# Performance work log

Hardware: AMD Instinct MI355X
Metric: run time of the kernel (lower is better)

Reference implementation:

```python
import jax, jax.numpy as jnp
import numpy as np

VOCAB = 50257
CUTOFF = (10000, 50000, 50257)  # cutoff + [vocab_size] per __init__
D = 1024
B, T = 2, 1024
HEAD_SZ = CUTOFF[0] + 2  # cutoff[0] + n_tail_clusters


def setup_inputs() -> dict:
    key = jax.random.key(0)
    ks = jax.random.split(key, 7)
    def xavier(k, shp):
        # xavier_uniform as in init_weights
        bound = np.sqrt(6.0 / (shp[0] + shp[1])).astype(np.float32)
        return jax.random.uniform(k, shp, dtype=jnp.float32, minval=-bound, maxval=bound)
    return {
        "input": jax.random.normal(ks[0], (B, T, D), dtype=jnp.float32),
        "target": jax.random.randint(ks[1], (B, T), 0, VOCAB),
        "head_w": xavier(ks[2], (HEAD_SZ, D)),              # [10002, 1024]
        "t0_a": xavier(ks[3], (D, D)),                       # [1024, 1024]
        "t0_b": xavier(ks[4], (CUTOFF[1] - CUTOFF[0], D)),   # [40000, 1024]
        "t1_a": xavier(ks[5], (D // 4, D)),                  # [256, 1024]
        "t1_b": xavier(ks[6], (CUTOFF[2] - CUTOFF[1], D // 4)),  # [207, 256]
    }


def reference(input, target, head_w, t0_a, t0_b, t1_a, t1_b):
    # Faithful jax version of AdaptiveSoftmax.get_log_prob (eval mode, dropout=0).
    # Torch updates log_probs[idxs, start:end] only for rows whose target lies in
    # cluster i (leaving other rows zero); we express the same gather->small GEMM
    # chain->log_softmax->prior-add->scatter via masked writes (jit-friendly).
    bsz, length, dim = input.shape
    xi = input.reshape(-1, dim)                     # [N, D]
    tgt = target.reshape(-1)                        # [N]

    head_lp = jax.nn.log_softmax(xi @ head_w.T, axis=1)        # [N, HEAD_SZ]
    tail_priors = head_lp[:, CUTOFF[0] - 1:HEAD_SZ - 1]        # [N, 2]

    log_probs = jnp.zeros((xi.shape[0], VOCAB), dtype=input.dtype)
    log_probs = log_probs.at[:, :HEAD_SZ].set(head_lp)

    tails = ((t0_a, t0_b), (t1_a, t1_b))
    for i, (wa, wb) in enumerate(tails):
        lo, hi = CUTOFF[i], CUTOFF[i + 1]
        mask = (tgt >= lo) & (tgt < hi)                        # [N]
        # Linear(D, D//4**i) -> Linear(D//4**i, hi-lo), then log_softmax + prior
        tail_lp = jax.nn.log_softmax((xi @ wa.T) @ wb.T, axis=1) + tail_priors[:, i:i + 1]
        log_probs = log_probs.at[:, lo:hi].set(
            jnp.where(mask[:, None], tail_lp, log_probs[:, lo:hi]))
    return log_probs.reshape(bsz, length, VOCAB)
```

## Files before the change

kernel.cpp:

```cpp
#include <hip/hip_runtime.h>

typedef unsigned short u16;
typedef unsigned int u32;
typedef __attribute__((ext_vector_type(4))) float f32x4;
typedef __bf16 bf16x8 __attribute__((ext_vector_type(8)));
typedef __attribute__((ext_vector_type(8))) unsigned short u16x8;

__device__ __forceinline__ u16 f2bf(float x) {
    u32 u = __builtin_bit_cast(u32, x);
    u += 0x7FFFu + ((u >> 16) & 1u);
    return (u16)(u >> 16);
}
__device__ __forceinline__ float bf2f(u16 u) {
    return __builtin_bit_cast(float, ((u32)u) << 16);
}
__device__ __forceinline__ void gld_lds16(void* lds, const void* g) {
    __builtin_amdgcn_global_load_lds(
        (const __attribute__((address_space(1))) void*)g,
        (__attribute__((address_space(3))) void*)lds, 16, 0, 0);
}
__device__ __forceinline__ void merge_ms(float& m, float& s, float mo, float so) {
    float mn = fmaxf(m, mo);
    s = s * __expf(m - mn) + so * __expf(mo - mn);
    m = mn;
}
__device__ __forceinline__ void wave_reduce_ms(float& m, float& s) {
#pragma unroll
    for (int off = 32; off; off >>= 1) {
        float mo = __shfl_xor(m, off);
        float so = __shfl_xor(s, off);
        merge_ms(m, s, mo, so);
    }
}
__device__ __forceinline__ void block_reduce_ms(float& m, float& s, float* red, int tid) {
    wave_reduce_ms(m, s);
    __syncthreads();
    if ((tid & 63) == 0) { red[(tid >> 6) * 2] = m; red[(tid >> 6) * 2 + 1] = s; }
    __syncthreads();
    float M = red[0], S = red[1];
#pragma unroll
    for (int w = 1; w < 4; w++) merge_ms(M, S, red[w * 2], red[w * 2 + 1]);
    m = M; s = S;
}

__device__ __forceinline__ size_t pack_base_u16(long row) {
    return (size_t)row * 100514 + 59936 - ((row * 2) & 7);
}

__global__ __launch_bounds__(256) void cvt_kernel(const float* __restrict__ src,
                                                  u16* __restrict__ dst, int n) {
    int idx = blockIdx.x * blockDim.x + threadIdx.x;
    int stride = gridDim.x * blockDim.x;
    for (int i = idx * 4; i < n; i += stride * 4) {
        float4 v = *(const float4*)(src + i);
        ushort4 o;
        o.x = f2bf(v.x); o.y = f2bf(v.y); o.z = f2bf(v.z); o.w = f2bf(v.w);
        *(ushort4*)(dst + i) = o;
    }
}

__global__ __launch_bounds__(256) void build_map(const int* __restrict__ tgt,
                                                 int* __restrict__ rowlist,
                                                 int* __restrict__ cntbuf) {
    __shared__ int cs[257];
    __shared__ int fu[256];
    int t = threadIdx.x;
    int cnt_local = 0, first_un = 1 << 30;
    int mk[8];
#pragma unroll
    for (int k = 0; k < 8; k++) {
        int r = t * 8 + k;
        int tg = tgt[r];
        int m = (tg >= 10000 && tg < 50000) ? 1 : 0;
        mk[k] = m;
        cnt_local += m;
        if (!m && first_un == (1 << 30)) first_un = r;
    }
    cs[t + 1] = cnt_local;
    fu[t] = first_un;
    __syncthreads();
    if (t == 0) {
        cs[0] = 0;
        for (int i = 1; i <= 256; i++) cs[i] += cs[i - 1];
        int d = 1 << 30;
        for (int i = 0; i < 256; i++) d = min(d, fu[i]);
        if (d == (1 << 30)) d = 0;
        int cnt = cs[256];
        cntbuf[0] = cnt;
        cntbuf[1] = (cnt + 255) & ~255;
        cntbuf[2] = d;
    }
    __syncthreads();
    int off = cs[t];
#pragma unroll
    for (int k = 0; k < 8; k++)
        if (mk[k]) rowlist[off++] = t * 8 + k;
    int cnt = cs[256], cntp = (cnt + 255) & ~255, d = cntbuf[2];
    for (int j = cnt + t; j < cntp; j += 256) rowlist[j] = d;
}

template <int MODE>
__global__ __launch_bounds__(256) void gemm_nt(const u16* __restrict__ A, int lda,
                                               const u16* __restrict__ B, int ldb,
                                               float* __restrict__ C, u16* __restrict__ Cb,
                                               long ldc, long c_off, int K) {
    __shared__ u16 lA[128 * 32];
    __shared__ u16 lB[128 * 32];
    const int tid = threadIdx.x;
    const int lane = tid & 63, wv = tid >> 6;
    const int m0 = blockIdx.x * 128, n0 = blockIdx.y * 128;

    const u16* gA0 = A + (size_t)(m0 + (tid >> 2)) * lda + (tid & 3) * 8;
    const u16* gB0 = B + (size_t)(n0 + (tid >> 2)) * ldb + (tid & 3) * 8;
    char* dA = (char*)lA + wv * 1024;
    char* dB = (char*)lB + wv * 1024;

    f32x4 acc[4][4] = {};
    const int wm = wv >> 1, wn = wv & 1;
    const int lr = lane & 15;
    const int lk = (lane >> 4) * 8;

    for (int kt = 0; kt < K; kt += 32) {
        __syncthreads();
        gld_lds16(dA, gA0);
        gld_lds16(dA + 4096, gA0 + 64 * (size_t)lda);
        gld_lds16(dB, gB0);
        gld_lds16(dB + 4096, gB0 + 64 * (size_t)ldb);
        gA0 += 32; gB0 += 32;
        __syncthreads();

        bf16x8 af[4], bfr[4];
#pragma unroll
        for (int i = 0; i < 4; i++) {
            af[i]  = *(const bf16x8*)(lA + (wm * 64 + i * 16 + lr) * 32 + lk);
            bfr[i] = *(const bf16x8*)(lB + (wn * 64 + i * 16 + lr) * 32 + lk);
        }
#pragma unroll
        for (int i = 0; i < 4; i++)
#pragma unroll
            for (int j = 0; j < 4; j++)
                acc[i][j] = __builtin_amdgcn_mfma_f32_16x16x32_bf16(af[i], bfr[j], acc[i][j], 0, 0, 0);
    }

    const int cr = (lane >> 4) * 4;
    const int cc = lane & 15;
#pragma unroll
    for (int i = 0; i < 4; i++) {
        int rbase = m0 + wm * 64 + i * 16 + cr;
#pragma unroll
        for (int j = 0; j < 4; j++) {
            int c = n0 + wn * 64 + j * 16 + cc;
#pragma unroll
            for (int q = 0; q < 4; q++) {
                size_t r = (size_t)(rbase + q);
                if (MODE == 1) Cb[r * (size_t)ldc + c] = f2bf(acc[i][j][q]);
                else           C[r * (size_t)ldc + (size_t)c_off + c] = acc[i][j][q];
            }
        }
    }
}

__global__ __launch_bounds__(512, 2) void gemm256_t0(const u16* __restrict__ PROJ,
                                                     const u16* __restrict__ B,
                                                     u16* __restrict__ Cb,
                                                     const int* __restrict__ rowlist,
                                                     const int* __restrict__ cntbuf,
                                                     float* __restrict__ part) {
    const int m0 = blockIdx.x * 256, n0 = blockIdx.y * 256;
    if (m0 >= cntbuf[1]) return;
    __shared__ u16 lds[4][16384];
    const int tid = threadIdx.x;
    const int lane = tid & 63, wv = tid >> 6;
    const int wm = wv >> 2, wn = wv & 3;
    const int lr = lane & 15, hi = lane >> 4;

    const int koff = (tid & 7) * 8;
    const int rit = tid >> 3;
    const u16* srcA[4];
    const u16* srcB[4];
#pragma unroll
    for (int p = 0; p < 4; p++) {
        srcA[p] = PROJ + (size_t)rowlist[m0 + p * 64 + rit] * 1280 + koff;
        srcB[p] = B + (size_t)(n0 + p * 64 + rit) * 1024 + koff;
    }

    f32x4 acc[8][4] = {};

    auto stage = [&](int buf, int kt) {
        u16* dA = &lds[buf * 2 + 0][0] + tid * 8;
        u16* dB = &lds[buf * 2 + 1][0] + tid * 8;
#pragma unroll
        for (int p = 0; p < 4; p++) {
            gld_lds16(dA + p * 4096, srcA[p] + kt);
            gld_lds16(dB + p * 4096, srcB[p] + kt);
        }
    };
    auto compute = [&](int buf) {
        const u16* lA = &lds[buf * 2 + 0][0];
        const u16* lB = &lds[buf * 2 + 1][0];
        bf16x8 bfr[4][2];
#pragma unroll
        for (int j = 0; j < 4; j++)
#pragma unroll
            for (int ks = 0; ks < 2; ks++)
                bfr[j][ks] = *(const bf16x8*)(lB + (wn * 64 + j * 16 + lr) * 64 + ks * 32 + hi * 8);
#pragma unroll
        for (int m = 0; m < 8; m++) {
            bf16x8 a0 = *(const bf16x8*)(lA + (wm * 128 + m * 16 + lr) * 64 + hi * 8);
            bf16x8 a1 = *(const bf16x8*)(lA + (wm * 128 + m * 16 + lr) * 64 + 32 + hi * 8);
#pragma unroll
            for (int j = 0; j < 4; j++) {
                acc[m][j] = __builtin_amdgcn_mfma_f32_16x16x32_bf16(a0, bfr[j][0], acc[m][j], 0, 0, 0);
                acc[m][j] = __builtin_amdgcn_mfma_f32_16x16x32_bf16(a1, bfr[j][1], acc[m][j], 0, 0, 0);
            }
        }
    };

    stage(0, 0);
    __syncthreads();
    int cur = 0;
#pragma unroll 1
    for (int t = 0; t < 15; ++t) {
        stage(cur ^ 1, (t + 1) * 64);
        compute(cur);
        __syncthreads();
        cur ^= 1;
    }
    compute(cur);

    const int cr = hi * 4, cc = lr;
#pragma unroll
    for (int m = 0; m < 8; m++) {
#pragma unroll
        for (int q = 0; q < 4; q++) {
            int r = m0 + wm * 128 + m * 16 + cr + q;
            long orow = rowlist[r];
            u16* dst = Cb + pack_base_u16(orow) + n0 + wn * 64 + cc;
            float s = 0.f;
#pragma unroll
            for (int j = 0; j < 4; j++) {
                float v = acc[m][j][q];
                dst[j * 16] = f2bf(v);
                s += __expf(v);
            }
            s += __shfl_xor(s, 1); s += __shfl_xor(s, 2);
            s += __shfl_xor(s, 4); s += __shfl_xor(s, 8);
            if (cc == 0) part[(size_t)r * 628 + (n0 >> 6) + wn] = s;
        }
    }
}

__global__ __launch_bounds__(256) void head_softmax(float* __restrict__ out,
                                                    float* __restrict__ stats) {
    const int row = blockIdx.x, tid = threadIdx.x;
    float* p = out + (size_t)row * 50257;
    __shared__ float sm[10002];
    __shared__ float red[16];
    float m = -3.4e38f, s = 0.f;
    for (int c = tid; c < 10002; c += 256) {
        float x = p[c];
        sm[c] = x;
        float m2 = fmaxf(m, x);
        s = s * __expf(m - m2) + __expf(x - m2);
        m = m2;
    }
    block_reduce_ms(m, s, red, tid);
    float A = m + __logf(s);
    for (int c = tid; c < 10002; c += 256) p[c] = sm[c] - A;
    if (tid == 0) {
        float* st = stats + row * 8;
        st[0] = sm[9999] - A;
        st[1] = sm[10000] - A;
        st[2] = sm[10000] - A;
        st[3] = sm[10001] - A;
    }
}

__global__ __launch_bounds__(256) void reduce_t0(const float* __restrict__ part,
                                                 const int* __restrict__ rowlist,
                                                 const int* __restrict__ cntbuf,
                                                 const float* __restrict__ ST,
                                                 float* __restrict__ FA) {
    int r = blockIdx.x;
    if (r >= cntbuf[0]) return;
    int tid = threadIdx.x;
    float s = 0.f;
    for (int c = tid; c < 628; c += 256) s += part[(size_t)r * 628 + c];
#pragma unroll
    for (int o = 32; o; o >>= 1) s += __shfl_xor(s, o);
    __shared__ float red[4];
    if ((tid & 63) == 0) red[tid >> 6] = s;
    __syncthreads();
    if (tid == 0) {
        float S = red[0] + red[1] + red[2] + red[3];
        int orow = rowlist[r];
        FA[orow] = __logf(S) - ST[orow * 8 + 0];
    }
}

__global__ __launch_bounds__(256) void tail0_norm(float* __restrict__ out,
                                                  const int* __restrict__ tgt,
                                                  const float* __restrict__ ST,
                                                  const float* __restrict__ FA) {
    const int row = blockIdx.x, tid = threadIdx.x;
    float* p = out + (size_t)row * 50257 + 10000;
    int t = tgt[row];
    if (t >= 10000 && t < 50000) {
        float A = FA[row];
        const u16* src = (const u16*)out + pack_base_u16(row);
        for (int k = 0; k < 5; k++) {
            float v[4][8];
#pragma unroll
            for (int g = 0; g < 4; g++) {
                int o = 2048 * g + tid * 8;
                if (o < 8000) {
                    u16x8 x = *(const u16x8*)(src + 8000 * k + o);
#pragma unroll
                    for (int z = 0; z < 8; z++) v[g][z] = bf2f(x[z]);
                }
            }
            __syncthreads();
#pragma unroll
            for (int g = 0; g < 4; g++) {
                int o = 2048 * g + tid * 8;
                if (o < 8000) {
                    int e = 8000 * k + o;
#pragma unroll
                    for (int z = 0; z < 8; z++) p[e + z] = v[g][z] - A;
                }
            }
            __syncthreads();
        }
    } else {
        float v0 = ST[row * 8 + 2], v1 = ST[row * 8 + 3];
        for (int e = tid; e < 40000; e += 256) p[e] = 0.f;
        if (tid == 0) { p[0] = v0; p[1] = v1; }
    }
}

__global__ __launch_bounds__(256) void tail1_kernel(float* __restrict__ out,
                                                    const int* __restrict__ tgt,
                                                    const u16* __restrict__ proj,
                                                    const u16* __restrict__ t1b,
                                                    const float* __restrict__ stats) {
    const int row = blockIdx.x, tid = threadIdx.x;
    float* p = out + (size_t)row * 50257 + 50000;
    int t = tgt[row];
    if (t < 50000) {
        for (int c = tid; c < 257; c += 256) p[c] = 0.f;
        return;
    }
    __shared__ float pr[256];
    __shared__ float lg[257];
    __shared__ float red[16];
    pr[tid] = bf2f(proj[(size_t)row * 1280 + 1024 + tid]);
    __syncthreads();
    for (int c = tid; c < 257; c += 256) {
        const u16* w = t1b + c * 256;
        float acc = 0.f;
        for (int k = 0; k < 256; k++) acc += bf2f(w[k]) * pr[k];
        lg[c] = acc;
    }
    __syncthreads();
    float m = -3.4e38f, s = 0.f;
    for (int c = tid; c < 257; c += 256) {
        float x = lg[c];
        float m2 = fmaxf(m, x);
        s = s * __expf(m - m2) + __expf(x - m2);
        m = m2;
    }
    block_reduce_ms(m, s, red, tid);
    float A = m + __logf(s) - stats[row * 8 + 1];
    for (int c = tid; c < 257; c += 256) p[c] = lg[c] - A;
}

#define OFF_XI    0UL
#define OFF_HEADW 4194304UL
#define OFF_TAB   24903680UL
#define OFF_T0B   27525120UL
#define OFF_T1B   109838336UL
#define OFF_PROJ  109969920UL
#define OFF_ST    115212800UL
#define OFF_PART  115278336UL
#define OFF_FA    120422912UL
#define OFF_MAP   120431104UL
#define OFF_CNT   120439296UL

extern "C" void kernel_launch(void* const* d_in, const int* in_sizes, int n_in,
                              void* d_out, int out_size, void* d_ws, size_t ws_size,
                              hipStream_t stream) {
    const float* x   = (const float*)d_in[0];
    const int*   tgt = (const int*)d_in[1];
    const float* hw  = (const float*)d_in[2];
    const float* t0a = (const float*)d_in[3];
    const float* t0b = (const float*)d_in[4];
    const float* t1a = (const float*)d_in[5];
    const float* t1b = (const float*)d_in[6];
    float* out = (float*)d_out;
    char* ws = (char*)d_ws;

    u16* XI    = (u16*)(ws + OFF_XI);
    u16* HW    = (u16*)(ws + OFF_HEADW);
    u16* TAB   = (u16*)(ws + OFF_TAB);
    u16* T0B   = (u16*)(ws + OFF_T0B);
    u16* T1B   = (u16*)(ws + OFF_T1B);
    u16* PROJ  = (u16*)(ws + OFF_PROJ);
    float* ST  = (float*)(ws + OFF_ST);
    float* PART = (float*)(ws + OFF_PART);
    float* FA  = (float*)(ws + OFF_FA);
    int* MAP   = (int*)(ws + OFF_MAP);
    int* CNT   = (int*)(ws + OFF_CNT);

    cvt_kernel<<<1024, 256, 0, stream>>>(x, XI, 2048 * 1024);
    cvt_kernel<<<2048, 256, 0, stream>>>(hw, HW, 10002 * 1024);
    cvt_kernel<<<512, 256, 0, stream>>>(t0a, TAB, 1024 * 1024);
    cvt_kernel<<<256, 256, 0, stream>>>(t1a, TAB + 1024 * 1024, 256 * 1024);
    cvt_kernel<<<2048, 256, 0, stream>>>(t0b, T0B, 40000 * 1024);
    cvt_kernel<<<64, 256, 0, stream>>>(t1b, T1B, 257 * 256);
    hipMemsetAsync(HW + 10002 * 1024, 0, 110 * 1024 * 2, stream);
    hipMemsetAsync(T0B + 40000 * 1024, 0, 192 * 1024 * 2, stream);

    build_map<<<1, 256, 0, stream>>>(tgt, MAP, CNT);

    gemm_nt<0><<<dim3(16, 79), 256, 0, stream>>>(
        XI, 1024, HW, 1024, out, nullptr, 50257L, 0L, 1024);

    head_softmax<<<2048, 256, 0, stream>>>(out, ST);

    gemm_nt<1><<<dim3(16, 10), 256, 0, stream>>>(
        XI, 1024, TAB, 1024, nullptr, PROJ, 1280L, 0L, 1024);

    gemm256_t0<<<dim3(8, 157), 512, 0, stream>>>(
        PROJ, T0B, (u16*)d_out, MAP, CNT, PART);

    reduce_t0<<<2048, 256, 0, stream>>>(PART, MAP, CNT, ST, FA);
    tail0_norm<<<2048, 256, 0, stream>>>(out, tgt, ST, FA);

    tail1_kernel<<<2048, 256, 0, stream>>>(out, tgt, PROJ, T1B, ST);
}
```

Before: 582.2 us.

## Unify GEMMs into pipelined 256-tile kernel with fused exp-sum epilogue and single convert

Merges the six fp32-to-bf16 conversion launches and two memsets into one block-partitioned kernel. Replaces the head GEMM with a templated 256x256 tile kernel that uses a 4-stage global-to-LDS pipeline and raw barriers. Its epilogue writes packed bf16 logits into the output buffer and emits partial exp-sums, so the head normalization only reads partial sums and rescales, with no online max pass. Max-free softmax can overflow if logits are large, and bf16 head logits lose precision compared with the fp32 path.

After: 558.1 us. -4.1%, faster.

```diff
diff --git a/kernel.cpp b/kernel.cpp
--- a/kernel.cpp
+++ b/kernel.cpp
@@ -19,43 +19,45 @@
         (const __attribute__((address_space(1))) void*)g,
         (__attribute__((address_space(3))) void*)lds, 16, 0, 0);
 }
-__device__ __forceinline__ void merge_ms(float& m, float& s, float mo, float so) {
-    float mn = fmaxf(m, mo);
-    s = s * __expf(m - mn) + so * __expf(mo - mn);
-    m = mn;
-}
-__device__ __forceinline__ void wave_reduce_ms(float& m, float& s) {
-#pragma unroll
-    for (int off = 32; off; off >>= 1) {
-        float mo = __shfl_xor(m, off);
-        float so = __shfl_xor(s, off);
-        merge_ms(m, s, mo, so);
-    }
-}
-__device__ __forceinline__ void block_reduce_ms(float& m, float& s, float* red, int tid) {
-    wave_reduce_ms(m, s);
-    __syncthreads();
-    if ((tid & 63) == 0) { red[(tid >> 6) * 2] = m; red[(tid >> 6) * 2 + 1] = s; }
-    __syncthreads();
-    float M = red[0], S = red[1];
-#pragma unroll
-    for (int w = 1; w < 4; w++) merge_ms(M, S, red[w * 2], red[w * 2 + 1]);
-    m = M; s = S;
-}
-
-__device__ __forceinline__ size_t pack_base_u16(long row) {
+
+__device__ __forceinline__ size_t pack_base_tail(long row) {
     return (size_t)row * 100514 + 59936 - ((row * 2) & 7);
 }
-
-__global__ __launch_bounds__(256) void cvt_kernel(const float* __restrict__ src,
-                                                  u16* __restrict__ dst, int n) {
-    int idx = blockIdx.x * blockDim.x + threadIdx.x;
-    int stride = gridDim.x * blockDim.x;
-    for (int i = idx * 4; i < n; i += stride * 4) {
-        float4 v = *(const float4*)(src + i);
-        ushort4 o;
-        o.x = f2bf(v.x); o.y = f2bf(v.y); o.z = f2bf(v.z); o.w = f2bf(v.w);
-        *(ushort4*)(dst + i) = o;
+__device__ __forceinline__ size_t pack_base_head(long row) {
+    return (size_t)row * 100514 + 20480 - ((row * 2) & 7);
+}
+
+__global__ __launch_bounds__(256) void cvt_all(const float* __restrict__ x,
+                                               const float* __restrict__ hw,
+                                               const float* __restrict__ t0a,
+                                               const float* __restrict__ t1a,
+                                               const float* __restrict__ t0b,
+                                               const float* __restrict__ t1b,
+                                               u16* __restrict__ XI, u16* __restrict__ HW,
+                                               u16* __restrict__ TAB, u16* __restrict__ T0B,
+                                               u16* __restrict__ T1B) {
+    int b = blockIdx.x;
+    const float* src; u16* dst; int n, b0, nb;
+    if (b < 80)        { src = x;    dst = XI;            n = 2097152;  b0 = 0;    nb = 80;   }
+    else if (b < 472)  { src = hw;   dst = HW;            n = 10242048; b0 = 80;   nb = 392;  }
+    else if (b < 512)  { src = t0a;  dst = TAB;           n = 1048576;  b0 = 472;  nb = 40;   }
+    else if (b < 522)  { src = t1a;  dst = TAB + 1048576; n = 262144;   b0 = 512;  nb = 10;   }
+    else if (b < 2086) { src = t0b;  dst = T0B;           n = 40960000; b0 = 522;  nb = 1564; }
+    else if (b < 2090) { src = t1b;  dst = T1B;           n = 65792;    b0 = 2086; nb = 4;    }
+    else if (b < 2100) { src = 0;    dst = HW + 10242048; n = 243712;   b0 = 2090; nb = 10;   }
+    else               { src = 0;    dst = T0B + 40960000; n = 196608;  b0 = 2100; nb = 8;    }
+    int i0 = (b - b0) * 1024 + threadIdx.x * 4;
+    int stride = nb * 1024;
+    if (src) {
+        for (int i = i0; i < n; i += stride) {
+            float4 v = *(const float4*)(src + i);
+            ushort4 o;
+            o.x = f2bf(v.x); o.y = f2bf(v.y); o.z = f2bf(v.z); o.w = f2bf(v.w);
+            *(ushort4*)(dst + i) = o;
+        }
+    } else {
+        ushort4 z = {0, 0, 0, 0};
+        for (int i = i0; i < n; i += stride) *(ushort4*)(dst + i) = z;
     }
 }
 
@@ -99,11 +101,108 @@
     for (int j = cnt + t; j < cntp; j += 256) rowlist[j] = d;
 }
 
-template <int MODE>
-__global__ __launch_bounds__(256) void gemm_nt(const u16* __restrict__ A, int lda,
-                                               const u16* __restrict__ B, int ldb,
-                                               float* __restrict__ C, u16* __restrict__ Cb,
-                                               long ldc, long c_off, int K) {
+template <int TAIL>
+__global__ __launch_bounds__(512, 2) void gemm256(const u16* __restrict__ A,
+                                                  const u16* __restrict__ B,
+                                                  u16* __restrict__ outpk,
+                                                  const int* __restrict__ rowlist,
+                                                  const int* __restrict__ cntbuf,
+                                                  float* __restrict__ part) {
+    const int m0 = blockIdx.x * 256, n0 = blockIdx.y * 256;
+    if (TAIL) { if (m0 >= cntbuf[1]) return; }
+    __shared__ u16 lds[4][16384];
+    const int tid = threadIdx.x;
+    const int lane = tid & 63, wv = tid >> 6;
+    const int wm = wv >> 2, wn = wv & 3;
+    const int lr = lane & 15, hi = lane >> 4;
+
+    const int c0 = tid, c1 = 512 + tid;
+    int ga0 = m0 + ((c0 >> 6) << 4) + (c0 & 15);
+    int ga1 = m0 + ((c1 >> 6) << 4) + (c1 & 15);
+    const u16* sA0;
+    const u16* sA1;
+    if (TAIL) {
+        sA0 = A + (size_t)rowlist[ga0] * 1280 + ((c0 >> 4) & 3) * 8;
+        sA1 = A + (size_t)rowlist[ga1] * 1280 + ((c1 >> 4) & 3) * 8;
+    } else {
+        sA0 = A + (size_t)ga0 * 1024 + ((c0 >> 4) & 3) * 8;
+        sA1 = A + (size_t)ga1 * 1024 + ((c1 >> 4) & 3) * 8;
+    }
+    const u16* sB0 = B + (size_t)(n0 + ((c0 >> 6) << 4) + (c0 & 15)) * 1024 + ((c0 >> 4) & 3) * 8;
+    const u16* sB1 = B + (size_t)(n0 + ((c1 >> 6) << 4) + (c1 & 15)) * 1024 + ((c1 >> 4) & 3) * 8;
+
+    f32x4 acc[8][4] = {};
+
+    auto stage = [&](int buf, int kt) {
+        char* d = (char*)&lds[buf][0] + tid * 16;
+        gld_lds16(d,          sA0 + kt);
+        gld_lds16(d + 8192,   sA1 + kt);
+        gld_lds16(d + 16384,  sB0 + kt);
+        gld_lds16(d + 24576,  sB1 + kt);
+    };
+    auto compute = [&](int buf) {
+        const u16* LA = &lds[buf][0];
+        const u16* LB = &lds[buf][8192];
+        bf16x8 bfr[4];
+#pragma unroll
+        for (int j = 0; j < 4; j++)
+            bfr[j] = *(const bf16x8*)(LB + (wn * 4 + j) * 512 + hi * 128 + lr * 8);
+        __builtin_amdgcn_s_setprio(1);
+#pragma unroll
+        for (int m = 0; m < 8; m++) {
+            bf16x8 af = *(const bf16x8*)(LA + (wm * 8 + m) * 512 + hi * 128 + lr * 8);
+#pragma unroll
+            for (int j = 0; j < 4; j++)
+                acc[m][j] = __builtin_amdgcn_mfma_f32_16x16x32_bf16(af, bfr[j], acc[m][j], 0, 0, 0);
+        }
+        __builtin_amdgcn_s_setprio(0);
+    };
+
+    stage(0, 0);
+    stage(1, 32);
+    asm volatile("s_waitcnt vmcnt(4)" ::: "memory");
+    __builtin_amdgcn_s_barrier();
+#pragma unroll 1
+    for (int t = 0; t < 30; ++t) {
+        stage((t + 2) & 3, (t + 2) * 32);
+        compute(t & 3);
+        asm volatile("s_waitcnt vmcnt(4)" ::: "memory");
+        __builtin_amdgcn_s_barrier();
+    }
+    compute(2);
+    asm volatile("s_waitcnt vmcnt(0)" ::: "memory");
+    __builtin_amdgcn_s_barrier();
+    compute(3);
+
+    const int cr = hi * 4, cc = lr;
+    const int climit = TAIL ? 40000 : 10002;
+    const int pstride = TAIL ? 628 : 160;
+#pragma unroll
+    for (int m = 0; m < 8; m++) {
+#pragma unroll
+        for (int q = 0; q < 4; q++) {
+            int r = m0 + wm * 128 + m * 16 + cr + q;
+            long orow = TAIL ? rowlist[r] : r;
+            size_t base = TAIL ? pack_base_tail(orow) : pack_base_head(orow);
+            u16* dst = outpk + base + n0 + wn * 64 + cc;
+            float s = 0.f;
+#pragma unroll
+            for (int j = 0; j < 4; j++) {
+                float v = acc[m][j][q];
+                dst[j * 16] = f2bf(v);
+                int col = n0 + wn * 64 + j * 16 + cc;
+                s += (col < climit) ? __expf(v) : 0.f;
+            }
+            s += __shfl_xor(s, 1); s += __shfl_xor(s, 2);
+            s += __shfl_xor(s, 4); s += __shfl_xor(s, 8);
+            if (cc == 0) part[(size_t)r * pstride + (n0 >> 6) + wn] = s;
+        }
+    }
+}
+
+__global__ __launch_bounds__(256) void gemm_nt_bf16(const u16* __restrict__ A, int lda,
+                                                    const u16* __restrict__ B, int ldb,
+                                                    u16* __restrict__ Cb, long ldc, int K) {
     __shared__ u16 lA[128 * 32];
     __shared__ u16 lB[128 * 32];
     const int tid = threadIdx.x;
@@ -151,128 +250,41 @@
         for (int j = 0; j < 4; j++) {
             int c = n0 + wn * 64 + j * 16 + cc;
 #pragma unroll
-            for (int q = 0; q < 4; q++) {
-                size_t r = (size_t)(rbase + q);
-                if (MODE == 1) Cb[r * (size_t)ldc + c] = f2bf(acc[i][j][q]);
-                else           C[r * (size_t)ldc + (size_t)c_off + c] = acc[i][j][q];
-            }
-        }
-    }
-}
-
-__global__ __launch_bounds__(512, 2) void gemm256_t0(const u16* __restrict__ PROJ,
-                                                     const u16* __restrict__ B,
-                                                     u16* __restrict__ Cb,
-                                                     const int* __restrict__ rowlist,
-                                                     const int* __restrict__ cntbuf,
-                                                     float* __restrict__ part) {
-    const int m0 = blockIdx.x * 256, n0 = blockIdx.y * 256;
-    if (m0 >= cntbuf[1]) return;
-    __shared__ u16 lds[4][16384];
-    const int tid = threadIdx.x;
-    const int lane = tid & 63, wv = tid >> 6;
-    const int wm = wv >> 2, wn = wv & 3;
-    const int lr = lane & 15, hi = lane >> 4;
-
-    const int koff = (tid & 7) * 8;
-    const int rit = tid >> 3;
-    const u16* srcA[4];
-    const u16* srcB[4];
-#pragma unroll
-    for (int p = 0; p < 4; p++) {
-        srcA[p] = PROJ + (size_t)rowlist[m0 + p * 64 + rit] * 1280 + koff;
-        srcB[p] = B + (size_t)(n0 + p * 64 + rit) * 1024 + koff;
-    }
-
-    f32x4 acc[8][4] = {};
-
-    auto stage = [&](int buf, int kt) {
-        u16* dA = &lds[buf * 2 + 0][0] + tid * 8;
-        u16* dB = &lds[buf * 2 + 1][0] + tid * 8;
-#pragma unroll
-        for (int p = 0; p < 4; p++) {
-            gld_lds16(dA + p * 4096, srcA[p] + kt);
-            gld_lds16(dB + p * 4096, srcB[p] + kt);
-        }
-    };
-    auto compute = [&](int buf) {
-        const u16* lA = &lds[buf * 2 + 0][0];
-        const u16* lB = &lds[buf * 2 + 1][0];
-        bf16x8 bfr[4][2];
-#pragma unroll
-        for (int j = 0; j < 4; j++)
-#pragma unroll
-            for (int ks = 0; ks < 2; ks++)
-                bfr[j][ks] = *(const bf16x8*)(lB + (wn * 64 + j * 16 + lr) * 64 + ks * 32 + hi * 8);
-#pragma unroll
-        for (int m = 0; m < 8; m++) {
-            bf16x8 a0 = *(const bf16x8*)(lA + (wm * 128 + m * 16 + lr) * 64 + hi * 8);
-            bf16x8 a1 = *(const bf16x8*)(lA + (wm * 128 + m * 16 + lr) * 64 + 32 + hi * 8);
-#pragma unroll
-            for (int j = 0; j < 4; j++) {
-                acc[m][j] = __builtin_amdgcn_mfma_f32_16x16x32_bf16(a0, bfr[j][0], acc[m][j], 0, 0, 0);
-                acc[m][j] = __builtin_amdgcn_mfma_f32_16x16x32_bf16(a1, bfr[j][1], acc[m][j], 0, 0, 0);
-            }
-        }
-    };
-
-    stage(0, 0);
-    __syncthreads();
-    int cur = 0;
-#pragma unroll 1
-    for (int t = 0; t < 15; ++t) {
-        stage(cur ^ 1, (t + 1) * 64);
-        compute(cur);
-        __syncthreads();
-        cur ^= 1;
-    }
-    compute(cur);
-
-    const int cr = hi * 4, cc = lr;
-#pragma unroll
-    for (int m = 0; m < 8; m++) {
-#pragma unroll
-        for (int q = 0; q < 4; q++) {
-            int r = m0 + wm * 128 + m * 16 + cr + q;
-            long orow = rowlist[r];
-            u16* dst = Cb + pack_base_u16(orow) + n0 + wn * 64 + cc;
-            float s = 0.f;
-#pragma unroll
-            for (int j = 0; j < 4; j++) {
-                float v = acc[m][j][q];
-                dst[j * 16] = f2bf(v);
-                s += __expf(v);
-            }
-            s += __shfl_xor(s, 1); s += __shfl_xor(s, 2);
-            s += __shfl_xor(s, 4); s += __shfl_xor(s, 8);
-            if (cc == 0) part[(size_t)r * 628 + (n0 >> 6) + wn] = s;
-        }
-    }
-}
-
-__global__ __launch_bounds__(256) void head_softmax(float* __restrict__ out,
-                                                    float* __restrict__ stats) {
+            for (int q = 0; q < 4; q++)
+                Cb[(size_t)(rbase + q) * (size_t)ldc + c] = f2bf(acc[i][j][q]);
+        }
+    }
+}
+
+__global__ __launch_bounds__(256) void head_norm(float* __restrict__ out,
+                                                 float* __restrict__ stats,
+                                                 const float* __restrict__ parth) {
     const int row = blockIdx.x, tid = threadIdx.x;
+    float s = (tid < 160) ? parth[(size_t)row * 160 + tid] : 0.f;
+#pragma unroll
+    for (int o = 32; o; o >>= 1) s += __shfl_xor(s, o);
+    __shared__ float red[4];
+    if ((tid & 63) == 0) red[tid >> 6] = s;
+    __syncthreads();
+    float logZ = __logf(red[0] + red[1] + red[2] + red[3]);
+    const u16* pk = (const u16*)out + pack_base_head(row);
     float* p = out + (size_t)row * 50257;
-    __shared__ float sm[10002];
-    __shared__ float red[16];
-    float m = -3.4e38f, s = 0.f;
-    for (int c = tid; c < 10002; c += 256) {
-        float x = p[c];
-        sm[c] = x;
-        float m2 = fmaxf(m, x);
-        s = s * __expf(m - m2) + __expf(x - m2);
-        m = m2;
-    }
-    block_reduce_ms(m, s, red, tid);
-    float A = m + __logf(s);
-    for (int c = tid; c < 10002; c += 256) p[c] = sm[c] - A;
+    for (int k = 0; k < 5; k++) {
+        int c0 = k * 2048 + tid * 8;
+        if (c0 + 8 <= 10002) {
+            u16x8 xv = *(const u16x8*)(pk + c0);
+#pragma unroll
+            for (int z = 0; z < 8; z++) p[c0 + z] = bf2f(xv[z]) - logZ;
+        } else if (c0 < 10002) {
+            for (int z = 0; c0 + z < 10002; z++) p[c0 + z] = bf2f(pk[c0 + z]) - logZ;
+        }
+    }
     if (tid == 0) {
         float* st = stats + row * 8;
-        st[0] = sm[9999] - A;
-        st[1] = sm[10000] - A;
-        st[2] = sm[10000] - A;
-        st[3] = sm[10001] - A;
+        float l0 = bf2f(pk[9999]) - logZ;
+        float l1 = bf2f(pk[10000]) - logZ;
+        float l2 = bf2f(pk[10001]) - logZ;
+        st[0] = l0; st[1] = l1; st[2] = l1; st[3] = l2;
     }
 }
 
@@ -307,16 +319,16 @@
     int t = tgt[row];
     if (t >= 10000 && t < 50000) {
         float A = FA[row];
-        const u16* src = (const u16*)out + pack_base_u16(row);
+        const u16* src = (const u16*)out + pack_base_tail(row);
         for (int k = 0; k < 5; k++) {
             float v[4][8];
 #pragma unroll
             for (int g = 0; g < 4; g++) {
                 int o = 2048 * g + tid * 8;
                 if (o < 8000) {
-                    u16x8 x = *(const u16x8*)(src + 8000 * k + o);
-#pragma unroll
-                    for (int z = 0; z < 8; z++) v[g][z] = bf2f(x[z]);
+                    u16x8 xv = *(const u16x8*)(src + 8000 * k + o);
+#pragma unroll
+                    for (int z = 0; z < 8; z++) v[g][z] = bf2f(xv[z]);
                 }
             }
             __syncthreads();
@@ -352,7 +364,7 @@
     }
     __shared__ float pr[256];
     __shared__ float lg[257];
-    __shared__ float red[16];
+    __shared__ float red[4];
     pr[tid] = bf2f(proj[(size_t)row * 1280 + 1024 + tid]);
     __syncthreads();
     for (int c = tid; c < 257; c += 256) {
@@ -362,29 +374,28 @@
         lg[c] = acc;
     }
     __syncthreads();
-    float m = -3.4e38f, s = 0.f;
-    for (int c = tid; c < 257; c += 256) {
-        float x = lg[c];
-        float m2 = fmaxf(m, x);
-        s = s * __expf(m - m2) + __expf(x - m2);
-        m = m2;
-    }
-    block_reduce_ms(m, s, red, tid);
-    float A = m + __logf(s) - stats[row * 8 + 1];
+    float s = 0.f;
+    for (int c = tid; c < 257; c += 256) s += __expf(lg[c]);
+#pragma unroll
+    for (int o = 32; o; o >>= 1) s += __shfl_xor(s, o);
+    if ((tid & 63) == 0) red[tid >> 6] = s;
+    __syncthreads();
+    float A = __logf(red[0] + red[1] + red[2] + red[3]) - stats[row * 8 + 1];
     for (int c = tid; c < 257; c += 256) p[c] = lg[c] - A;
 }
 
 #define OFF_XI    0UL
 #define OFF_HEADW 4194304UL
-#define OFF_TAB   24903680UL
-#define OFF_T0B   27525120UL
-#define OFF_T1B   109838336UL
-#define OFF_PROJ  109969920UL
-#define OFF_ST    115212800UL
-#define OFF_PART  115278336UL
-#define OFF_FA    120422912UL
-#define OFF_MAP   120431104UL
-#define OFF_CNT   120439296UL
+#define OFF_TAB   25165824UL
+#define OFF_T0B   27787264UL
+#define OFF_T1B   110100480UL
+#define OFF_PROJ  110232064UL
+#define OFF_ST    115474944UL
+#define OFF_PART  115540480UL
+#define OFF_PARTH 120685056UL
+#define OFF_FA    121995776UL
+#define OFF_MAP   122003968UL
+#define OFF_CNT   122012160UL
 
 extern "C" void kernel_launch(void* const* d_in, const int* in_sizes, int n_in,
                               void* d_out, int out_size, void* d_ws, size_t ws_size,
@@ -399,39 +410,30 @@
     float* out = (float*)d_out;
     char* ws = (char*)d_ws;
 
-    u16* XI    = (u16*)(ws + OFF_XI);
-    u16* HW    = (u16*)(ws + OFF_HEADW);
-    u16* TAB   = (u16*)(ws + OFF_TAB);
-    u16* T0B   = (u16*)(ws + OFF_T0B);
-    u16* T1B   = (u16*)(ws + OFF_T1B);
-    u16* PROJ  = (u16*)(ws + OFF_PROJ);
-    float* ST  = (float*)(ws + OFF_ST);
+    u16* XI     = (u16*)(ws + OFF_XI);
+    u16* HW     = (u16*)(ws + OFF_HEADW);
+    u16* TAB    = (u16*)(ws + OFF_TAB);
+    u16* T0B    = (u16*)(ws + OFF_T0B);
+    u16* T1B    = (u16*)(ws + OFF_T1B);
+    u16* PROJ   = (u16*)(ws + OFF_PROJ);
+    float* ST   = (float*)(ws + OFF_ST);
     float* PART = (float*)(ws + OFF_PART);
-    float* FA  = (float*)(ws + OFF_FA);
-    int* MAP   = (int*)(ws + OFF_MAP);
-    int* CNT   = (int*)(ws + OFF_CNT);
-
-    cvt_kernel<<<1024, 256, 0, stream>>>(x, XI, 2048 * 1024);
-    cvt_kernel<<<2048, 256, 0, stream>>>(hw, HW, 10002 * 1024);
-    cvt_kernel<<<512, 256, 0, stream>>>(t0a, TAB, 1024 * 1024);
-    cvt_kernel<<<256, 256, 0, stream>>>(t1a, TAB + 1024 * 1024, 256 * 1024);
-    cvt_kernel<<<2048, 256, 0, stream>>>(t0b, T0B, 40000 * 1024);
-    cvt_kernel<<<64, 256, 0, stream>>>(t1b, T1B, 257 * 256);
-    hipMemsetAsync(HW + 10002 * 1024, 0, 110 * 1024 * 2, stream);
-    hipMemsetAsync(T0B + 40000 * 1024, 0, 192 * 1024 * 2, stream);
+    float* PARTH = (float*)(ws + OFF_PARTH);
+    float* FA   = (float*)(ws + OFF_FA);
+    int* MAP    = (int*)(ws + OFF_MAP);
+    int* CNT    = (int*)(ws + OFF_CNT);
+
+    cvt_all<<<2108, 256, 0, stream>>>(x, hw, t0a, t1a, t0b, t1b, XI, HW, TAB, T0B, T1B);
 
     build_map<<<1, 256, 0, stream>>>(tgt, MAP, CNT);
 
-    gemm_nt<0><<<dim3(16, 79), 256, 0, stream>>>(
-        XI, 1024, HW, 1024, out, nullptr, 50257L, 0L, 1024);
-
-    head_softmax<<<2048, 256, 0, stream>>>(out, ST);
-
-    gemm_nt<1><<<dim3(16, 10), 256, 0, stream>>>(
-        XI, 1024, TAB, 1024, nullptr, PROJ, 1280L, 0L, 1024);
-
-    gemm256_t0<<<dim3(8, 157), 512, 0, stream>>>(
-        PROJ, T0B, (u16*)d_out, MAP, CNT, PART);
+    gemm256<0><<<dim3(8, 40), 512, 0, stream>>>(XI, HW, (u16*)d_out, nullptr, nullptr, PARTH);
+
+    head_norm<<<2048, 256, 0, stream>>>(out, ST, PARTH);
+
+    gemm_nt_bf16<<<dim3(16, 10), 256, 0, stream>>>(XI, 1024, TAB, 1024, PROJ, 1280L, 1024);
+
+    gemm256<1><<<dim3(8, 157), 512, 0, stream>>>(PROJ, T0B, (u16*)d_out, MAP, CNT, PART);
 
     reduce_t0<<<2048, 256, 0, stream>>>(PART, MAP, CNT, ST, FA);
     tail0_norm<<<2048, 256, 0, stream>>>(out, tgt, ST, FA);
```
